# Kernel tuning notes

Hardware: AMD Instinct MI355X
Metric: run time of the kernel (lower is better)

## Reference

```python
import jax, jax.numpy as jnp
import numpy as np

B, T, D, H = 64, 512, 1024, 1024


def setup_inputs() -> dict:
    key = jax.random.key(0)
    ks = jax.random.split(key, 9)
    s_in = 1.0 / np.sqrt(D + H)  # torch Linear default init scale
    inp = {
        "x": jax.random.normal(ks[0], (B, T, D), dtype=jnp.float32),
        "Wi": jax.random.uniform(ks[1], (H, D + H), jnp.float32, -s_in, s_in),
        "bi": jax.random.uniform(ks[2], (H,), jnp.float32, -s_in, s_in),
        "Wf": jax.random.uniform(ks[3], (H, D + H), jnp.float32, -s_in, s_in),
        "bf": jax.random.uniform(ks[4], (H,), jnp.float32, -s_in, s_in),
        "Wo": jax.random.uniform(ks[5], (H, D + H), jnp.float32, -s_in, s_in),
        "bo": jax.random.uniform(ks[6], (H,), jnp.float32, -s_in, s_in),
        "Wc": jax.random.uniform(ks[7], (H, D + H), jnp.float32, -s_in, s_in),
        "bc": jax.random.uniform(ks[8], (H,), jnp.float32, -s_in, s_in),
    }
    return inp


def reference(x, Wi, bi, Wf, bf, Wo, bo, Wc, bc):
    # x: [B, T, D]; returns stacked hidden states [T, B, H]
    batch = x.shape[0]
    hidden = Wi.shape[0]
    h0 = jnp.zeros((batch, hidden), dtype=x.dtype)
    c0 = jnp.zeros((batch, hidden), dtype=x.dtype)

    def step(carry, x_t):
        h, c = carry
        inp = jnp.concatenate([x_t, h], axis=1)  # [B, D+H]
        f = jax.nn.sigmoid(inp @ Wf.T + bf)
        i = jax.nn.sigmoid(inp @ Wi.T + bi)
        o = jax.nn.sigmoid(inp @ Wo.T + bo)
        g = jnp.tanh(inp @ Wc.T + bc)
        c_new = f * c + i * g
        h_new = o * jnp.tanh(c_new)
        return (h_new, c_new), h_new

    xs = jnp.transpose(x, (1, 0, 2))  # [T, B, D]
    _, h_states = jax.lax.scan(step, (h0, c0), xs)
    return h_states  # [T, B, H]
```

## Files before the change

kernel.cpp:

```cpp
#include <hip/hip_runtime.h>


typedef short short8 __attribute__((ext_vector_type(8)));
typedef float f32x4 __attribute__((ext_vector_type(4)));

#define NBLK 128
#define TPB 256

__device__ __forceinline__ unsigned bfbits(float f) {
  unsigned u = __float_as_uint(f);
  return ((u + 0x7fffu + ((u >> 16) & 1u)) >> 16) & 0xffffu;
}

__device__ __forceinline__ short8 cvt8(const float* p) {
  const float4* q = (const float4*)p;
  float4 a = q[0], b = q[1];
  short8 r;
  r[0] = (short)bfbits(a.x); r[1] = (short)bfbits(a.y);
  r[2] = (short)bfbits(a.z); r[3] = (short)bfbits(a.w);
  r[4] = (short)bfbits(b.x); r[5] = (short)bfbits(b.y);
  r[6] = (short)bfbits(b.z); r[7] = (short)bfbits(b.w);
  return r;
}

__device__ __forceinline__ short8 llc_load16(const unsigned short* p) {
  short8 r;
  asm volatile("global_load_dwordx4 %0, %1, off sc0 sc1"
               : "=v"(r)
               : "v"(p));
  return r;
}

__device__ __forceinline__ float sigmoidf_(float x) {
  return 1.0f / (1.0f + __expf(-x));
}
__device__ __forceinline__ float tanhf_(float x) {
  float ax = fabsf(x);
  float e = __expf(-2.0f * ax);
  float r = (1.0f - e) / (1.0f + e);
  return copysignf(r, x);
}

__global__ void cvt_x_kernel(const float* __restrict__ x,
                             unsigned short* __restrict__ xb, int n4) {
  int i = blockIdx.x * blockDim.x + threadIdx.x;
  int stride = gridDim.x * blockDim.x;
  const float4* xv = (const float4*)x;
  uint2* ov = (uint2*)xb;
  for (; i < n4; i += stride) {
    float4 v = xv[i];
    uint2 o;
    o.x = bfbits(v.x) | (bfbits(v.y) << 16);
    o.y = bfbits(v.z) | (bfbits(v.w) << 16);
    ov[i] = o;
  }
}

__global__ __launch_bounds__(TPB, 1) void lstm_persist(
    const float* __restrict__ x, const unsigned short* __restrict__ xb,
    const float* __restrict__ Wi, const float* __restrict__ Wf,
    const float* __restrict__ Wo, const float* __restrict__ Wc,
    const float* __restrict__ bi, const float* __restrict__ bfv,
    const float* __restrict__ bo, const float* __restrict__ bc,
    unsigned short* __restrict__ hbuf, unsigned* __restrict__ cnt,
    float* __restrict__ out) {
  constexpr int B = 64, T = 512, D = 1024, H = 1024;
  const int tid = threadIdx.x;
  const int bid = blockIdx.x;
  const int lane = tid & 63;
  const int w = tid >> 6;
  const int cl = lane & 15;
  const int kg = lane >> 4;
  const int j0 = bid * 8;

  __shared__ float part[4][32][68];

  const float* Wg[4] = {Wi, Wf, Wo, Wc};
  short8 bxw[2][8], bhw[2][8];
#pragma unroll
  for (int nt = 0; nt < 2; ++nt) {
    int g = 2 * nt + (cl >> 3);
    const float* wrow = Wg[g] + (size_t)(j0 + (cl & 7)) * 2048;
#pragma unroll
    for (int kf = 0; kf < 8; ++kf) {
      int kx = 256 * w + 32 * kf + 8 * kg;
      bxw[nt][kf] = cvt8(wrow + kx);
      bhw[nt][kf] = cvt8(wrow + 1024 + kx);
    }
  }

  const int row = tid >> 2;
  const int up = tid & 3;
  float biasv[4][2];
#pragma unroll
  for (int k = 0; k < 2; ++k) {
    biasv[0][k] = bi[j0 + 2 * up + k];
    biasv[1][k] = bfv[j0 + 2 * up + k];
    biasv[2][k] = bo[j0 + 2 * up + k];
    biasv[3][k] = bc[j0 + 2 * up + k];
  }
  float cst[2] = {0.0f, 0.0f};

  unsigned* hz = (unsigned*)(hbuf + 65536);
  __hip_atomic_store(&hz[bid * TPB + tid], 0u, __ATOMIC_RELAXED,
                     __HIP_MEMORY_SCOPE_AGENT);
  __syncthreads();
  if (tid == 0)
    __hip_atomic_fetch_add(cnt, 1u, __ATOMIC_RELAXED, __HIP_MEMORY_SCOPE_AGENT);

  const int kxbase = 256 * w + 8 * kg;

  for (int t = 0; t < T; ++t) {
    const unsigned short* hprev = hbuf + (((t & 1) ^ 1) * 65536);
    unsigned short* hnext = hbuf + ((t & 1) * 65536);

    f32x4 acc[4][2];
#pragma unroll
    for (int mt = 0; mt < 4; ++mt)
#pragma unroll
      for (int nt = 0; nt < 2; ++nt) acc[mt][nt] = (f32x4)0.0f;

#pragma unroll
    for (int kf = 0; kf < 8; ++kf) {
      int kx = kxbase + 32 * kf;
      short8 af[4];
      if (xb) {
#pragma unroll
        for (int mt = 0; mt < 4; ++mt) {
          int b = 16 * mt + cl;
          af[mt] = *(const short8*)(xb + ((size_t)b * T + t) * D + kx);
        }
      } else {
#pragma unroll
        for (int mt = 0; mt < 4; ++mt) {
          int b = 16 * mt + cl;
          af[mt] = cvt8(x + ((size_t)b * T + t) * D + kx);
        }
      }
#pragma unroll
      for (int mt = 0; mt < 4; ++mt) {
        acc[mt][0] = __builtin_amdgcn_mfma_f32_16x16x32_bf16(
            af[mt], bxw[0][kf], acc[mt][0], 0, 0, 0);
        acc[mt][1] = __builtin_amdgcn_mfma_f32_16x16x32_bf16(
            af[mt], bxw[1][kf], acc[mt][1], 0, 0, 0);
      }
    }

    const unsigned target = (unsigned)NBLK * (unsigned)(t + 1);
    if (tid == 0) {
      while (__hip_atomic_load(cnt, __ATOMIC_RELAXED,
                               __HIP_MEMORY_SCOPE_AGENT) < target)
        __builtin_amdgcn_s_sleep(1);
    }
    __syncthreads();
    asm volatile("" ::: "memory");

    short8 ah[8][4];
#pragma unroll
    for (int kf = 0; kf < 8; ++kf) {
      int kh = kxbase + 32 * kf;
#pragma unroll
      for (int mt = 0; mt < 4; ++mt)
        ah[kf][mt] = llc_load16(hprev + (16 * mt + cl) * H + kh);
    }
    asm volatile("s_waitcnt vmcnt(0)" ::: "memory");
    __builtin_amdgcn_sched_barrier(0);

#pragma unroll
    for (int kf = 0; kf < 8; ++kf) {
#pragma unroll
      for (int mt = 0; mt < 4; ++mt) {
        acc[mt][0] = __builtin_amdgcn_mfma_f32_16x16x32_bf16(
            ah[kf][mt], bhw[0][kf], acc[mt][0], 0, 0, 0);
        acc[mt][1] = __builtin_amdgcn_mfma_f32_16x16x32_bf16(
            ah[kf][mt], bhw[1][kf], acc[mt][1], 0, 0, 0);
      }
    }

#pragma unroll
    for (int mt = 0; mt < 4; ++mt)
#pragma unroll
      for (int nt = 0; nt < 2; ++nt)
        *(f32x4*)&part[w][16 * nt + cl][16 * mt + 4 * kg] = acc[mt][nt];
    __syncthreads();

    float hv[2];
#pragma unroll
    for (int k = 0; k < 2; ++k) {
      int u = 2 * up + k;
      float pre[4];
#pragma unroll
      for (int g = 0; g < 4; ++g) {
        float s = biasv[g][k];
#pragma unroll
        for (int ww = 0; ww < 4; ++ww) s += part[ww][8 * g + u][row];
        pre[g] = s;
      }
      float iv = sigmoidf_(pre[0]);
      float fv = sigmoidf_(pre[1]);
      float ov = sigmoidf_(pre[2]);
      float gv = tanhf_(pre[3]);
      cst[k] = fv * cst[k] + iv * gv;
      hv[k] = ov * tanhf_(cst[k]);
    }
    unsigned hpack = bfbits(hv[0]) | (bfbits(hv[1]) << 16);
    __hip_atomic_store((unsigned*)(hnext + row * H + j0 + 2 * up), hpack,
                       __ATOMIC_RELAXED, __HIP_MEMORY_SCOPE_AGENT);
    float2 o2 = make_float2(hv[0], hv[1]);
    *(float2*)(out + ((size_t)t * B + row) * H + j0 + 2 * up) = o2;

    __syncthreads();
    asm volatile("" ::: "memory");
    if (tid == 0)
      __hip_atomic_fetch_add(cnt, 1u, __ATOMIC_RELAXED,
                             __HIP_MEMORY_SCOPE_AGENT);
  }
}

extern "C" void kernel_launch(void* const* d_in, const int* in_sizes, int n_in,
                              void* d_out, int out_size, void* d_ws,
                              size_t ws_size, hipStream_t stream) {
  const float* x = (const float*)d_in[0];
  const float* Wi = (const float*)d_in[1];
  const float* bi = (const float*)d_in[2];
  const float* Wf = (const float*)d_in[3];
  const float* bfv = (const float*)d_in[4];
  const float* Wo = (const float*)d_in[5];
  const float* bo = (const float*)d_in[6];
  const float* Wc = (const float*)d_in[7];
  const float* bc = (const float*)d_in[8];
  float* out = (float*)d_out;

  char* ws = (char*)d_ws;
  const size_t xb_bytes = (size_t)64 * 512 * 1024 * 2;
  const size_t small_bytes = (size_t)2 * 64 * 1024 * 2 + 256;
  unsigned short* xb = nullptr;
  size_t off = 0;
  if (ws_size >= xb_bytes + small_bytes) {
    xb = (unsigned short*)ws;
    off = xb_bytes;
  }
  unsigned short* hbuf = (unsigned short*)(ws + off);
  off += (size_t)2 * 64 * 1024 * 2;
  unsigned* cnt = (unsigned*)(ws + off);

  hipMemsetAsync(cnt, 0, sizeof(unsigned), stream);
  if (xb) cvt_x_kernel<<<2048, 256, 0, stream>>>(x, xb, (64 * 512 * 1024) / 4);
  lstm_persist<<<NBLK, TPB, 0, stream>>>(x, xb, Wi, Wf, Wo, Wc, bi, bfv, bo, bc,
                                         hbuf, cnt, out);
}
```

Before: 4.799 ms.

## Replace atomic counter barrier with per-block flags and pipeline h loads with MFMAs

The single global atomic counter that every block incremented each step is replaced with per-block flag words padded to separate cache lines. Wave 0 of each block polls all 128 flags in parallel and uses a wave vote to detect completion. The h-state loads now use a scalar base plus immediate offsets, and staged waitcnts let the MFMAs start on the first chunks while later chunks are still in flight. The output store moves after the flag release and becomes nontemporal, taking it off the critical path. Polling 128 flags adds memory traffic during the spin, and the correctness of the barrier now depends on the flag ordering.

```diff
diff --git a/kernel.cpp b/kernel.cpp
--- a/kernel.cpp
+++ b/kernel.cpp
@@ -23,11 +23,13 @@
   return r;
 }
 
-__device__ __forceinline__ short8 llc_load16(const unsigned short* p) {
+template <int OFF>
+__device__ __forceinline__ short8 llc_load16s(const unsigned short* base,
+                                              int voff) {
   short8 r;
-  asm volatile("global_load_dwordx4 %0, %1, off sc0 sc1"
+  asm volatile("global_load_dwordx4 %0, %1, %2 offset:%3 sc0 sc1"
                : "=v"(r)
-               : "v"(p));
+               : "v"(voff), "s"(base), "n"(OFF));
   return r;
 }
 
@@ -62,7 +64,7 @@
     const float* __restrict__ Wo, const float* __restrict__ Wc,
     const float* __restrict__ bi, const float* __restrict__ bfv,
     const float* __restrict__ bo, const float* __restrict__ bc,
-    unsigned short* __restrict__ hbuf, unsigned* __restrict__ cnt,
+    unsigned short* __restrict__ hbuf, unsigned* __restrict__ flags,
     float* __restrict__ out) {
   constexpr int B = 64, T = 512, D = 1024, H = 1024;
   const int tid = threadIdx.x;
@@ -101,14 +103,19 @@
   }
   float cst[2] = {0.0f, 0.0f};
 
+  const int kxbase = 256 * w + 8 * kg;
+  int voff[4];
+#pragma unroll
+  for (int mt = 0; mt < 4; ++mt)
+    voff[mt] = (((16 * mt + cl) << 10) + kxbase) * 2;
+
   unsigned* hz = (unsigned*)(hbuf + 65536);
   __hip_atomic_store(&hz[bid * TPB + tid], 0u, __ATOMIC_RELAXED,
                      __HIP_MEMORY_SCOPE_AGENT);
   __syncthreads();
   if (tid == 0)
-    __hip_atomic_fetch_add(cnt, 1u, __ATOMIC_RELAXED, __HIP_MEMORY_SCOPE_AGENT);
-
-  const int kxbase = 256 * w + 8 * kg;
+    __hip_atomic_store(&flags[bid * 32], 1u, __ATOMIC_RELAXED,
+                       __HIP_MEMORY_SCOPE_AGENT);
 
   for (int t = 0; t < T; ++t) {
     const unsigned short* hprev = hbuf + (((t & 1) ^ 1) * 65536);
@@ -146,36 +153,46 @@
       }
     }
 
-    const unsigned target = (unsigned)NBLK * (unsigned)(t + 1);
-    if (tid == 0) {
-      while (__hip_atomic_load(cnt, __ATOMIC_RELAXED,
-                               __HIP_MEMORY_SCOPE_AGENT) < target)
+    const unsigned target = (unsigned)(t + 1);
+    if (w == 0) {
+      const unsigned* f0 = flags + (2 * lane) * 32;
+      const unsigned* f1 = flags + (2 * lane + 1) * 32;
+      while (true) {
+        unsigned a = __hip_atomic_load(f0, __ATOMIC_RELAXED,
+                                       __HIP_MEMORY_SCOPE_AGENT);
+        unsigned b = __hip_atomic_load(f1, __ATOMIC_RELAXED,
+                                       __HIP_MEMORY_SCOPE_AGENT);
+        if (__all(a >= target && b >= target)) break;
         __builtin_amdgcn_s_sleep(1);
+      }
     }
     __syncthreads();
     asm volatile("" ::: "memory");
 
     short8 ah[8][4];
-#pragma unroll
-    for (int kf = 0; kf < 8; ++kf) {
-      int kh = kxbase + 32 * kf;
-#pragma unroll
-      for (int mt = 0; mt < 4; ++mt)
-        ah[kf][mt] = llc_load16(hprev + (16 * mt + cl) * H + kh);
-    }
-    asm volatile("s_waitcnt vmcnt(0)" ::: "memory");
-    __builtin_amdgcn_sched_barrier(0);
-
-#pragma unroll
-    for (int kf = 0; kf < 8; ++kf) {
-#pragma unroll
-      for (int mt = 0; mt < 4; ++mt) {
-        acc[mt][0] = __builtin_amdgcn_mfma_f32_16x16x32_bf16(
-            ah[kf][mt], bhw[0][kf], acc[mt][0], 0, 0, 0);
-        acc[mt][1] = __builtin_amdgcn_mfma_f32_16x16x32_bf16(
-            ah[kf][mt], bhw[1][kf], acc[mt][1], 0, 0, 0);
-      }
-    }
+#define HLOAD(kf)                                         \
+  ah[kf][0] = llc_load16s<64 * (kf)>(hprev, voff[0]);     \
+  ah[kf][1] = llc_load16s<64 * (kf)>(hprev, voff[1]);     \
+  ah[kf][2] = llc_load16s<64 * (kf)>(hprev, voff[2]);     \
+  ah[kf][3] = llc_load16s<64 * (kf)>(hprev, voff[3]);
+    HLOAD(0) HLOAD(1) HLOAD(2) HLOAD(3)
+    HLOAD(4) HLOAD(5) HLOAD(6) HLOAD(7)
+#undef HLOAD
+
+#define HMFMA(kf, rem)                                                      \
+  asm volatile("s_waitcnt vmcnt(" #rem ")" ::: "memory");                   \
+  __builtin_amdgcn_sched_barrier(0);                                        \
+  {                                                                         \
+    _Pragma("unroll") for (int mt = 0; mt < 4; ++mt) {                      \
+      acc[mt][0] = __builtin_amdgcn_mfma_f32_16x16x32_bf16(                 \
+          ah[kf][mt], bhw[0][kf], acc[mt][0], 0, 0, 0);                     \
+      acc[mt][1] = __builtin_amdgcn_mfma_f32_16x16x32_bf16(                 \
+          ah[kf][mt], bhw[1][kf], acc[mt][1], 0, 0, 0);                     \
+    }                                                                       \
+  }
+    HMFMA(0, 28) HMFMA(1, 24) HMFMA(2, 20) HMFMA(3, 16)
+    HMFMA(4, 12) HMFMA(5, 8) HMFMA(6, 4) HMFMA(7, 0)
+#undef HMFMA
 
 #pragma unroll
     for (int mt = 0; mt < 4; ++mt)
@@ -206,14 +223,16 @@
     unsigned hpack = bfbits(hv[0]) | (bfbits(hv[1]) << 16);
     __hip_atomic_store((unsigned*)(hnext + row * H + j0 + 2 * up), hpack,
                        __ATOMIC_RELAXED, __HIP_MEMORY_SCOPE_AGENT);
-    float2 o2 = make_float2(hv[0], hv[1]);
-    *(float2*)(out + ((size_t)t * B + row) * H + j0 + 2 * up) = o2;
 
     __syncthreads();
     asm volatile("" ::: "memory");
     if (tid == 0)
-      __hip_atomic_fetch_add(cnt, 1u, __ATOMIC_RELAXED,
-                             __HIP_MEMORY_SCOPE_AGENT);
+      __hip_atomic_store(&flags[bid * 32], (unsigned)(t + 2), __ATOMIC_RELAXED,
+                         __HIP_MEMORY_SCOPE_AGENT);
+
+    float* op = out + ((size_t)t * B + row) * H + j0 + 2 * up;
+    __builtin_nontemporal_store(hv[0], op);
+    __builtin_nontemporal_store(hv[1], op + 1);
   }
 }
 
@@ -233,19 +252,20 @@
 
   char* ws = (char*)d_ws;
   const size_t xb_bytes = (size_t)64 * 512 * 1024 * 2;
-  const size_t small_bytes = (size_t)2 * 64 * 1024 * 2 + 256;
+  const size_t hb_bytes = (size_t)2 * 64 * 1024 * 2;
+  const size_t fl_bytes = (size_t)NBLK * 32 * 4;
   unsigned short* xb = nullptr;
   size_t off = 0;
-  if (ws_size >= xb_bytes + small_bytes) {
+  if (ws_size >= xb_bytes + hb_bytes + fl_bytes) {
     xb = (unsigned short*)ws;
     off = xb_bytes;
   }
   unsigned short* hbuf = (unsigned short*)(ws + off);
-  off += (size_t)2 * 64 * 1024 * 2;
-  unsigned* cnt = (unsigned*)(ws + off);
-
-  hipMemsetAsync(cnt, 0, sizeof(unsigned), stream);
+  off += hb_bytes;
+  unsigned* flags = (unsigned*)(ws + off);
+
+  hipMemsetAsync(flags, 0, fl_bytes, stream);
   if (xb) cvt_x_kernel<<<2048, 256, 0, stream>>>(x, xb, (64 * 512 * 1024) / 4);
   lstm_persist<<<NBLK, TPB, 0, stream>>>(x, xb, Wi, Wf, Wo, Wc, bi, bfv, bo, bc,
-                                         hbuf, cnt, out);
-}
+                                         hbuf, flags, out);
+}
```

After: 4.450 ms. 7.3% less time.

## Replace global counter barrier with per-block flags and full h history buffer

Applied to the files above, without the earlier changes.

Swaps the single atomic counter grid barrier for per-block padded flag words, which every wave polls in parallel with a wave-wide vote. The ping-pong h buffer becomes a history buffer with one slot per timestep, so h loads can be plain cached loads instead of LLC-bypassing ones. The flag is raised before the output store, and the output store becomes nontemporal, taking it off the critical path. This removes atomic contention and the block-wide syncthreads before h reads, at the cost of about 67MB of workspace. Plain loads rely on never reading a stale cached address, since each slot is written only once.

```diff
diff --git a/kernel.cpp b/kernel.cpp
--- a/kernel.cpp
+++ b/kernel.cpp
@@ -20,14 +20,6 @@
   r[2] = (short)bfbits(a.z); r[3] = (short)bfbits(a.w);
   r[4] = (short)bfbits(b.x); r[5] = (short)bfbits(b.y);
   r[6] = (short)bfbits(b.z); r[7] = (short)bfbits(b.w);
-  return r;
-}
-
-__device__ __forceinline__ short8 llc_load16(const unsigned short* p) {
-  short8 r;
-  asm volatile("global_load_dwordx4 %0, %1, off sc0 sc1"
-               : "=v"(r)
-               : "v"(p));
   return r;
 }
 
@@ -62,7 +54,7 @@
     const float* __restrict__ Wo, const float* __restrict__ Wc,
     const float* __restrict__ bi, const float* __restrict__ bfv,
     const float* __restrict__ bo, const float* __restrict__ bc,
-    unsigned short* __restrict__ hbuf, unsigned* __restrict__ cnt,
+    unsigned short* __restrict__ hist, unsigned* __restrict__ flags,
     float* __restrict__ out) {
   constexpr int B = 64, T = 512, D = 1024, H = 1024;
   const int tid = threadIdx.x;
@@ -73,6 +65,8 @@
   const int kg = lane >> 4;
   const int j0 = bid * 8;
 
+  __builtin_amdgcn_fence(__ATOMIC_ACQUIRE, "agent");
+
   __shared__ float part[4][32][68];
 
   const float* Wg[4] = {Wi, Wf, Wo, Wc};
@@ -101,18 +95,19 @@
   }
   float cst[2] = {0.0f, 0.0f};
 
-  unsigned* hz = (unsigned*)(hbuf + 65536);
+  const int kxbase = 256 * w + 8 * kg;
+
+  unsigned* hz = (unsigned*)hist;
   __hip_atomic_store(&hz[bid * TPB + tid], 0u, __ATOMIC_RELAXED,
                      __HIP_MEMORY_SCOPE_AGENT);
   __syncthreads();
   if (tid == 0)
-    __hip_atomic_fetch_add(cnt, 1u, __ATOMIC_RELAXED, __HIP_MEMORY_SCOPE_AGENT);
-
-  const int kxbase = 256 * w + 8 * kg;
+    __hip_atomic_store(&flags[bid * 32], 1u, __ATOMIC_RELAXED,
+                       __HIP_MEMORY_SCOPE_AGENT);
 
   for (int t = 0; t < T; ++t) {
-    const unsigned short* hprev = hbuf + (((t & 1) ^ 1) * 65536);
-    unsigned short* hnext = hbuf + ((t & 1) * 65536);
+    const unsigned short* hprev = hist + (size_t)t * 65536;
+    unsigned short* hnext = hist + (size_t)(t + 1) * 65536;
 
     f32x4 acc[4][2];
 #pragma unroll
@@ -146,13 +141,16 @@
       }
     }
 
-    const unsigned target = (unsigned)NBLK * (unsigned)(t + 1);
-    if (tid == 0) {
-      while (__hip_atomic_load(cnt, __ATOMIC_RELAXED,
-                               __HIP_MEMORY_SCOPE_AGENT) < target)
+    {
+      const unsigned target = (unsigned)(t + 1);
+      const unsigned* fp = flags + (size_t)(32 * w + (lane & 31)) * 32;
+      while (true) {
+        unsigned v =
+            __hip_atomic_load(fp, __ATOMIC_RELAXED, __HIP_MEMORY_SCOPE_AGENT);
+        if (__all((int)(v >= target))) break;
         __builtin_amdgcn_s_sleep(1);
-    }
-    __syncthreads();
+      }
+    }
     asm volatile("" ::: "memory");
 
     short8 ah[8][4];
@@ -161,11 +159,8 @@
       int kh = kxbase + 32 * kf;
 #pragma unroll
       for (int mt = 0; mt < 4; ++mt)
-        ah[kf][mt] = llc_load16(hprev + (16 * mt + cl) * H + kh);
-    }
-    asm volatile("s_waitcnt vmcnt(0)" ::: "memory");
-    __builtin_amdgcn_sched_barrier(0);
-
+        ah[kf][mt] = *(const short8*)(hprev + (size_t)(16 * mt + cl) * H + kh);
+    }
 #pragma unroll
     for (int kf = 0; kf < 8; ++kf) {
 #pragma unroll
@@ -204,16 +199,18 @@
       hv[k] = ov * tanhf_(cst[k]);
     }
     unsigned hpack = bfbits(hv[0]) | (bfbits(hv[1]) << 16);
-    __hip_atomic_store((unsigned*)(hnext + row * H + j0 + 2 * up), hpack,
-                       __ATOMIC_RELAXED, __HIP_MEMORY_SCOPE_AGENT);
-    float2 o2 = make_float2(hv[0], hv[1]);
-    *(float2*)(out + ((size_t)t * B + row) * H + j0 + 2 * up) = o2;
+    __hip_atomic_store((unsigned*)(hnext + (size_t)row * H + j0 + 2 * up),
+                       hpack, __ATOMIC_RELAXED, __HIP_MEMORY_SCOPE_AGENT);
 
     __syncthreads();
     asm volatile("" ::: "memory");
     if (tid == 0)
-      __hip_atomic_fetch_add(cnt, 1u, __ATOMIC_RELAXED,
-                             __HIP_MEMORY_SCOPE_AGENT);
+      __hip_atomic_store(&flags[bid * 32], (unsigned)(t + 2), __ATOMIC_RELAXED,
+                         __HIP_MEMORY_SCOPE_AGENT);
+
+    float* op = out + ((size_t)t * B + row) * H + j0 + 2 * up;
+    __builtin_nontemporal_store(hv[0], op);
+    __builtin_nontemporal_store(hv[1], op + 1);
   }
 }
 
@@ -233,19 +230,21 @@
 
   char* ws = (char*)d_ws;
   const size_t xb_bytes = (size_t)64 * 512 * 1024 * 2;
-  const size_t small_bytes = (size_t)2 * 64 * 1024 * 2 + 256;
+  const size_t hist_bytes = (size_t)513 * 64 * 1024 * 2;
+  const size_t fl_bytes = (size_t)NBLK * 32 * 4;
+
   unsigned short* xb = nullptr;
   size_t off = 0;
-  if (ws_size >= xb_bytes + small_bytes) {
+  if (ws_size >= xb_bytes + hist_bytes + fl_bytes) {
     xb = (unsigned short*)ws;
     off = xb_bytes;
   }
-  unsigned short* hbuf = (unsigned short*)(ws + off);
-  off += (size_t)2 * 64 * 1024 * 2;
-  unsigned* cnt = (unsigned*)(ws + off);
-
-  hipMemsetAsync(cnt, 0, sizeof(unsigned), stream);
+  unsigned short* hist = (unsigned short*)(ws + off);
+  off += hist_bytes;
+  unsigned* flags = (unsigned*)(ws + off);
+
+  hipMemsetAsync(flags, 0, fl_bytes, stream);
   if (xb) cvt_x_kernel<<<2048, 256, 0, stream>>>(x, xb, (64 * 512 * 1024) / 4);
   lstm_persist<<<NBLK, TPB, 0, stream>>>(x, xb, Wi, Wf, Wo, Wc, bi, bfv, bo, bc,
-                                         hbuf, cnt, out);
-}
+                                         hist, flags, out);
+}
```

Measured after the change: 4.507 ms. 1.06x faster.
